# Performance work log

Hardware: AMD Instinct MI355X
Metric: run time of the kernel (lower is better)

Reference implementation:

```python
import jax, jax.numpy as jnp
import numpy as np

B = 16          # graphs per batch
N_PER = 1024    # coarse points per graph
M_PER = 4096    # fine (skip) points per graph
K = 3           # knn neighbors
NVEC = 64       # number of l=1 (vector) reps -> F = 3*NVEC
F = 3 * NVEC
F_SKIP = 64
HID = 256
OUT = 128
N = B * N_PER
M = B * M_PER


def _random_rotations(key, n):
    # QR of gaussian -> orthonormal local frames [n,3,3]
    q, _ = jnp.linalg.qr(jax.random.normal(key, (n, 3, 3), dtype=jnp.float32))
    return q


def setup_inputs() -> dict:
    key = jax.random.key(0)
    ks = jax.random.split(key, 10)
    x = jax.random.normal(ks[0], (N, F), dtype=jnp.float32)
    pos = jax.random.normal(ks[1], (N, 3), dtype=jnp.float32)
    pos_skip = jax.random.normal(ks[2], (M, 3), dtype=jnp.float32)
    x_skip = jax.random.normal(ks[3], (M, F_SKIP), dtype=jnp.float32)
    lframes = _random_rotations(ks[4], N)
    lframes_skip = _random_rotations(ks[5], M)
    W1 = jax.random.normal(ks[6], (F + F_SKIP, HID), dtype=jnp.float32) * 0.05
    b1 = jnp.zeros((HID,), dtype=jnp.float32)
    W2 = jax.random.normal(ks[7], (HID, OUT), dtype=jnp.float32) * 0.05
    b2 = jnp.zeros((OUT,), dtype=jnp.float32)
    batch = jnp.repeat(jnp.arange(B, dtype=jnp.int64), N_PER)
    batch_skip = jnp.repeat(jnp.arange(B, dtype=jnp.int64), M_PER)
    return dict(x=x, pos=pos, pos_skip=pos_skip, x_skip=x_skip,
                lframes=lframes, lframes_skip=lframes_skip,
                W1=W1, b1=b1, W2=W2, b2=b2,
                batch=batch, batch_skip=batch_skip)


def _knn_indices(pos, pos_skip):
    # Uniform per-example batching: knn of fine points (queries) among coarse points.
    px = pos.reshape(B, N_PER, 3)       # source points
    py = pos_skip.reshape(B, M_PER, 3)  # query points
    # squared distances via ||y||^2 + ||x||^2 - 2 y.x (only used for ranking)
    d2 = ((py * py).sum(-1)[:, :, None]
          + (px * px).sum(-1)[:, None, :]
          - 2.0 * jnp.einsum('bmd,bnd->bmn', py, px))  # [B, M_PER, N_PER]
    _, idx = jax.lax.top_k(-d2, K)                     # [B, M_PER, K] local indices
    # globalize indices (batch offset)
    x_idx = (idx + (jnp.arange(B) * N_PER)[:, None, None]).reshape(M, K)
    return x_idx


def reference(x, pos, pos_skip, x_skip, lframes, lframes_skip,
              W1, b1, W2, b2, batch, batch_skip):
    x_idx = _knn_indices(pos, pos_skip)                 # [M, K]

    # exact squared distances on gathered neighbors (matches torch diff*diff path)
    diff = pos[x_idx] - pos_skip[:, None, :]            # [M, K, 3]
    sqd = (diff * diff).sum(-1)                         # [M, K]
    w = 1.0 / jnp.maximum(sqd, 1e-16)                   # [M, K]

    # change of local frames: U = R_end @ R_start^T, per edge
    Rx = lframes[x_idx]                                 # [M, K, 3, 3]
    Ry = lframes_skip                                   # [M, 3, 3]
    U = jnp.einsum('mab,mkcb->mkac', Ry, Rx)            # [M, K, 3, 3]

    # transform features (NVEC vector reps) into the target frame
    xv = x[x_idx].reshape(M, K, NVEC, 3)                # gathered edge features
    xt = jnp.einsum('mkab,mkvb->mkva', U, xv)           # [M, K, NVEC, 3]

    # weighted mean over the K neighbors (== scatter-sum / scatter-sum, since
    # each target node has exactly K incoming edges)
    num = (xt * w[:, :, None, None]).sum(axis=1)        # [M, NVEC, 3]
    den = w.sum(axis=1)[:, None, None]                  # [M, 1, 1]
    y = (num / den).reshape(M, F)

    h = jnp.concatenate([y, x_skip], axis=-1)           # [M, F + F_SKIP]
    out = jax.nn.relu(h @ W1 + b1) @ W2 + b2            # [M, OUT]
    return (out, pos_skip, batch_skip, lframes_skip)
```

## Files before the change

### kernel.cpp

```cpp
#include <hip/hip_runtime.h>
#include <hip/hip_bf16.h>

#define B_GR   16
#define N_PER  1024
#define M_PER  4096
#define NVEC   64
#define FDIM   192
#define FSKIP  64
#define HID    256
#define ODIM   128
#define N_TOT  (B_GR * N_PER)
#define M_TOT  (B_GR * M_PER)

typedef __attribute__((ext_vector_type(8))) short short8v;
typedef __attribute__((ext_vector_type(4))) float f32x4;

__device__ __forceinline__ unsigned short f2bf(float f) {
    __hip_bfloat16 h = __float2bfloat16(f);
    return *reinterpret_cast<unsigned short*>(&h);
}

__device__ __forceinline__ int hsw(int r, int e) {
    return r * 256 + (e ^ ((r & 7) << 3));
}

__global__ __launch_bounds__(256) void prep_tail_kernel(
    const float* __restrict__ W1, const float* __restrict__ W2,
    const float* __restrict__ pos_skip,
    const int*   __restrict__ batch_skip,
    const float* __restrict__ lframes_skip,
    unsigned short* __restrict__ wt1, unsigned short* __restrict__ wt2,
    float* __restrict__ dst)
{
    const int i = blockIdx.x * 256 + threadIdx.x;
    if (i < 65536) {
        const int k = i >> 8, c = i & 255;
        wt1[c * 256 + k] = f2bf(W1[i]);
    } else if (i < 98304) {
        const int j = i - 65536;
        const int k = j >> 7, c = j & 127;
        wt2[c * 256 + k] = f2bf(W2[j]);
    } else {
        const int t = i - 98304;
        const int P = M_TOT * 3;
        const int Q = P + M_TOT;
        if (t < P)      dst[t] = pos_skip[t];
        else if (t < Q) dst[t] = (float)batch_skip[t - P];
        else            dst[t] = lframes_skip[t - Q];
    }
}

__global__ __launch_bounds__(512, 2) void fused_kernel(
    const float* __restrict__ x,
    const float* __restrict__ pos,
    const float* __restrict__ pos_skip,
    const float* __restrict__ x_skip,
    const float* __restrict__ lframes,
    const float* __restrict__ lframes_skip,
    const unsigned short* __restrict__ wt1,
    const float* __restrict__ b1,
    const unsigned short* __restrict__ wt2,
    const float* __restrict__ b2,
    float* __restrict__ out)
{
    __shared__ __align__(16) char smraw[64 * 256 * 2];
    __shared__ __align__(16) float Usc[64 * 28];
    __shared__ int idxL[64 * 3];

    float4*         pc = reinterpret_cast<float4*>(smraw);
    unsigned short* hb = reinterpret_cast<unsigned short*>(smraw);

    const int tid  = threadIdx.x;
    const int lane = tid & 63;
    const int wv   = tid >> 6;
    const int raw  = blockIdx.x;
    const int blk  = (raw & 7) * 128 + (raw >> 3);
    const int lo   = lane & 15;
    const int hi   = lane >> 4;
    const int b    = blk >> 6;

    #pragma unroll
    for (int k = 0; k < 2; ++k) {
        const int j = tid + k * 512;
        const float* p = pos + (size_t)(b * N_PER + j) * 3;
        float a0 = p[0], a1 = p[1], a2 = p[2];
        pc[j] = make_float4(a0, a1, a2, a0*a0 + a1*a1 + a2*a2);
    }
    __syncthreads();

    {
        const int q   = tid >> 3;
        const int sub = tid & 7;
        const int m   = blk * 64 + q;
        float nqx, nqy, nqz, qq;
        {
            const float qx = pos_skip[m*3+0], qy = pos_skip[m*3+1],
                        qz = pos_skip[m*3+2];
            qq  = qx*qx + qy*qy + qz*qz;
            nqx = -2.0f*qx; nqy = -2.0f*qy; nqz = -2.0f*qz;
        }

        float d0 = 1e30f, d1 = 1e30f, d2 = 1e30f;
        int   i0 = 0,     i1 = 0,     i2 = 0;
        #pragma unroll 4
        for (int t = 0; t < 128; ++t) {
            const int j = t*8 + sub;
            float4 c = pc[j];
            float r = fmaf(nqx, c.x, fmaf(nqy, c.y, fmaf(nqz, c.z, qq + c.w)));
            bool c0 = r < d0, c1 = r < d1, c2 = r < d2;
            i2 = c2 ? (c1 ? i1 : j) : i2;
            i1 = c1 ? (c0 ? i0 : j) : i1;
            i0 = c0 ? j : i0;
            d2 = c2 ? (c1 ? d1 : r) : d2;
            d1 = c1 ? (c0 ? d0 : r) : d1;
            d0 = c0 ? r : d0;
        }
        #pragma unroll
        for (int mask = 1; mask <= 4; mask <<= 1) {
            float e0 = __shfl_xor(d0, mask), e1 = __shfl_xor(d1, mask),
                  e2 = __shfl_xor(d2, mask);
            int   j0 = __shfl_xor(i0, mask), j1 = __shfl_xor(i1, mask),
                  j2 = __shfl_xor(i2, mask);
            const float ee[3] = {e0, e1, e2};
            const int   jj[3] = {j0, j1, j2};
            #pragma unroll
            for (int s = 0; s < 3; ++s) {
                const float e = ee[s]; const int j = jj[s];
                bool c0 = (e < d0) || (e == d0 && j < i0);
                bool c1 = (e < d1) || (e == d1 && j < i1);
                bool c2 = (e < d2) || (e == d2 && j < i2);
                i2 = c2 ? (c1 ? i1 : j) : i2;
                i1 = c1 ? (c0 ? i0 : j) : i1;
                i0 = c0 ? j : i0;
                d2 = c2 ? (c1 ? d1 : e) : d2;
                d1 = c1 ? (c0 ? d0 : e) : d1;
                d0 = c0 ? e : d0;
            }
        }

        if (sub < 3) {
            const int jl = (sub == 0) ? i0 : (sub == 1) ? i1 : i2;
            idxL[q*3 + sub] = jl;

            const float qx = -0.5f*nqx, qy = -0.5f*nqy, qz = -0.5f*nqz;
            float w[3];
            const int jls[3] = {i0, i1, i2};
            #pragma unroll
            for (int s = 0; s < 3; ++s) {
                float4 c = pc[jls[s]];
                float dx = c.x - qx, dy = c.y - qy, dz = c.z - qz;
                w[s] = 1.0f / fmaxf(dx*dx + dy*dy + dz*dz, 1e-16f);
            }
            const float wsub = (sub == 0) ? w[0] : (sub == 1) ? w[1] : w[2];
            const float sS   = wsub / (w[0] + w[1] + w[2]);
            const int   nb   = b * N_PER + jl;

            float RyS[9], Rx[9];
            #pragma unroll
            for (int t = 0; t < 9; ++t) RyS[t] = sS * lframes_skip[(size_t)m*9 + t];
            #pragma unroll
            for (int t = 0; t < 9; ++t) Rx[t] = lframes[(size_t)nb*9 + t];

            float* dst = &Usc[q*28 + sub*9];
            #pragma unroll
            for (int a = 0; a < 3; ++a)
                #pragma unroll
                for (int c = 0; c < 3; ++c)
                    dst[a*3+c] = RyS[a*3+0]*Rx[c*3+0]
                               + RyS[a*3+1]*Rx[c*3+1]
                               + RyS[a*3+2]*Rx[c*3+2];
        }
    }

    if (wv >= 4) {
        #pragma unroll
        for (int rr = 0; rr < 8; ++rr) {
            const int r = wv * 8 + rr;
            const int m = blk * 64 + r;
            hb[hsw(r, 192+lane)] = f2bf(x_skip[(size_t)m*FSKIP + lane]);
        }
    }
    __syncthreads();

    for (int rr = 0; rr < 8; ++rr) {
        const int r = wv * 8 + rr;
        const int m = blk * 64 + r;
        const int nbs[3] = {b*N_PER + idxL[r*3+0],
                            b*N_PER + idxL[r*3+1],
                            b*N_PER + idxL[r*3+2]};

        float Ub[28];
        float4* Ub4 = reinterpret_cast<float4*>(Ub);
        #pragma unroll
        for (int t = 0; t < 7; ++t)
            Ub4[t] = *reinterpret_cast<const float4*>(&Usc[r*28 + t*4]);

        float n0 = 0.f, n1 = 0.f, n2 = 0.f;
        #pragma unroll
        for (int k = 0; k < 3; ++k) {
            const float* xp = x + (size_t)nbs[k]*FDIM + lane*3;
            const float v0 = xp[0], v1 = xp[1], v2 = xp[2];
            const int o = k*9;
            n0 += Ub[o+0]*v0 + Ub[o+1]*v1 + Ub[o+2]*v2;
            n1 += Ub[o+3]*v0 + Ub[o+4]*v1 + Ub[o+5]*v2;
            n2 += Ub[o+6]*v0 + Ub[o+7]*v1 + Ub[o+8]*v2;
        }
        hb[hsw(r, lane*3+0)] = f2bf(n0);
        hb[hsw(r, lane*3+1)] = f2bf(n1);
        hb[hsw(r, lane*3+2)] = f2bf(n2);
        if (wv < 4)
            hb[hsw(r, 192+lane)] = f2bf(x_skip[(size_t)m*FSKIP + lane]);
    }
    __syncthreads();

    f32x4 acc[4][2];
    #pragma unroll
    for (int fi = 0; fi < 4; ++fi)
        #pragma unroll
        for (int ci = 0; ci < 2; ++ci) acc[fi][ci] = (f32x4)0.f;

    for (int ks = 0; ks < 8; ++ks) {
        const int kk = ks*32 + hi*8;
        short8v a[4], bf[2];
        #pragma unroll
        for (int fi = 0; fi < 4; ++fi) {
            const int r = fi*16 + lo;
            a[fi] = *reinterpret_cast<const short8v*>(
                &hb[r*256 + (kk ^ ((lo & 7) << 3))]);
        }
        #pragma unroll
        for (int ci = 0; ci < 2; ++ci) {
            const int cb = wv*32 + ci*16 + lo;
            bf[ci] = *reinterpret_cast<const short8v*>(&wt1[cb*256 + kk]);
        }
        #pragma unroll
        for (int fi = 0; fi < 4; ++fi)
            #pragma unroll
            for (int ci = 0; ci < 2; ++ci)
                acc[fi][ci] = __builtin_amdgcn_mfma_f32_16x16x32_bf16(
                    a[fi], bf[ci], acc[fi][ci], 0, 0, 0);
    }
    __syncthreads();

    {
        float b1v[2];
        #pragma unroll
        for (int ci = 0; ci < 2; ++ci) b1v[ci] = b1[wv*32 + ci*16 + lo];
        #pragma unroll
        for (int fi = 0; fi < 4; ++fi)
            #pragma unroll
            for (int ci = 0; ci < 2; ++ci)
                #pragma unroll
                for (int q = 0; q < 4; ++q) {
                    const int r = fi*16 + hi*4 + q;
                    const int c = wv*32 + ci*16 + lo;
                    hb[hsw(r, c)] = f2bf(fmaxf(acc[fi][ci][q] + b1v[ci], 0.f));
                }
    }
    __syncthreads();

    f32x4 acc2[4];
    #pragma unroll
    for (int fi = 0; fi < 4; ++fi) acc2[fi] = (f32x4)0.f;

    for (int ks = 0; ks < 8; ++ks) {
        const int kk = ks*32 + hi*8;
        short8v a[4], bf;
        #pragma unroll
        for (int fi = 0; fi < 4; ++fi) {
            const int r = fi*16 + lo;
            a[fi] = *reinterpret_cast<const short8v*>(
                &hb[r*256 + (kk ^ ((lo & 7) << 3))]);
        }
        {
            const int cb = wv*16 + lo;
            bf = *reinterpret_cast<const short8v*>(&wt2[cb*256 + kk]);
        }
        #pragma unroll
        for (int fi = 0; fi < 4; ++fi)
            acc2[fi] = __builtin_amdgcn_mfma_f32_16x16x32_bf16(
                a[fi], bf, acc2[fi], 0, 0, 0);
    }

    {
        const float b2v = b2[wv*16 + lo];
        #pragma unroll
        for (int fi = 0; fi < 4; ++fi)
            #pragma unroll
            for (int q = 0; q < 4; ++q) {
                const int r = fi*16 + hi*4 + q;
                const int c = wv*16 + lo;
                out[(size_t)(blk*64 + r)*ODIM + c] = acc2[fi][q] + b2v;
            }
    }
}

extern "C" void kernel_launch(void* const* d_in, const int* in_sizes, int n_in,
                              void* d_out, int out_size, void* d_ws, size_t ws_size,
                              hipStream_t stream) {
    const float* x            = (const float*)d_in[0];
    const float* pos          = (const float*)d_in[1];
    const float* pos_skip     = (const float*)d_in[2];
    const float* x_skip       = (const float*)d_in[3];
    const float* lframes      = (const float*)d_in[4];
    const float* lframes_skip = (const float*)d_in[5];
    const float* W1           = (const float*)d_in[6];
    const float* b1           = (const float*)d_in[7];
    const float* W2           = (const float*)d_in[8];
    const float* b2           = (const float*)d_in[9];
    const int*   batch_skip   = (const int*)d_in[11];

    char* ws = (char*)d_ws;
    unsigned short* wt1 = (unsigned short*)ws;
    unsigned short* wt2 = (unsigned short*)(ws + 131072);
    float* out  = (float*)d_out;
    float* tail = out + (size_t)M_TOT * ODIM;

    prep_tail_kernel<<<3712, 256, 0, stream>>>(W1, W2, pos_skip, batch_skip,
                                               lframes_skip, wt1, wt2, tail);

    fused_kernel<<<M_TOT/64, 512, 0, stream>>>(x, pos, pos_skip, x_skip,
                                               lframes, lframes_skip,
                                               wt1, b1, wt2, b2, out);
}
```

Measured before the change: 66.26 us.

## Split fused kernel into separate kNN and MLP kernels

The kNN search moves out of the fused kernel into its own kernel, which writes global neighbor indices to workspace. The MLP kernel reads those indices, recomputes the weights from global pos, and loads x_skip up front. The goal is to give each phase its own occupancy and register budget, with the kNN kernel declared for 4 blocks per CU. The cost is an extra launch, a round trip of the indices through global memory, and the loss of overlap between the two phases inside one block.

After: 78.79 us. 1.19x slower.

```diff
diff --git a/kernel.cpp b/kernel.cpp
--- a/kernel.cpp
+++ b/kernel.cpp
@@ -50,7 +50,81 @@
     }
 }
 
-__global__ __launch_bounds__(512, 2) void fused_kernel(
+__global__ __launch_bounds__(512, 4) void knn_kernel(
+    const float* __restrict__ pos,
+    const float* __restrict__ pos_skip,
+    int* __restrict__ idxb)
+{
+    __shared__ float4 pc[N_PER];
+    const int tid = threadIdx.x;
+    const int raw = blockIdx.x;
+    const int blk = (raw & 7) * 128 + (raw >> 3);
+    const int b   = blk >> 6;
+
+    #pragma unroll
+    for (int k = 0; k < 2; ++k) {
+        const int j = tid + k * 512;
+        const float* p = pos + (size_t)(b * N_PER + j) * 3;
+        float a0 = p[0], a1 = p[1], a2 = p[2];
+        pc[j] = make_float4(a0, a1, a2, a0*a0 + a1*a1 + a2*a2);
+    }
+    __syncthreads();
+
+    const int q   = tid >> 3;
+    const int sub = tid & 7;
+    const int m   = blk * 64 + q;
+    float nqx, nqy, nqz, qq;
+    {
+        const float qx = pos_skip[m*3+0], qy = pos_skip[m*3+1],
+                    qz = pos_skip[m*3+2];
+        qq  = qx*qx + qy*qy + qz*qz;
+        nqx = -2.0f*qx; nqy = -2.0f*qy; nqz = -2.0f*qz;
+    }
+
+    float d0 = 1e30f, d1 = 1e30f, d2 = 1e30f;
+    int   i0 = 0,     i1 = 0,     i2 = 0;
+    #pragma unroll 4
+    for (int t = 0; t < 128; ++t) {
+        const int j = t*8 + sub;
+        float4 c = pc[j];
+        float r = fmaf(nqx, c.x, fmaf(nqy, c.y, fmaf(nqz, c.z, qq + c.w)));
+        bool c0 = r < d0, c1 = r < d1, c2 = r < d2;
+        i2 = c2 ? (c1 ? i1 : j) : i2;
+        i1 = c1 ? (c0 ? i0 : j) : i1;
+        i0 = c0 ? j : i0;
+        d2 = c2 ? (c1 ? d1 : r) : d2;
+        d1 = c1 ? (c0 ? d0 : r) : d1;
+        d0 = c0 ? r : d0;
+    }
+    #pragma unroll
+    for (int mask = 1; mask <= 4; mask <<= 1) {
+        float e0 = __shfl_xor(d0, mask), e1 = __shfl_xor(d1, mask),
+              e2 = __shfl_xor(d2, mask);
+        int   j0 = __shfl_xor(i0, mask), j1 = __shfl_xor(i1, mask),
+              j2 = __shfl_xor(i2, mask);
+        const float ee[3] = {e0, e1, e2};
+        const int   jj[3] = {j0, j1, j2};
+        #pragma unroll
+        for (int s = 0; s < 3; ++s) {
+            const float e = ee[s]; const int j = jj[s];
+            bool c0 = (e < d0) || (e == d0 && j < i0);
+            bool c1 = (e < d1) || (e == d1 && j < i1);
+            bool c2 = (e < d2) || (e == d2 && j < i2);
+            i2 = c2 ? (c1 ? i1 : j) : i2;
+            i1 = c1 ? (c0 ? i0 : j) : i1;
+            i0 = c0 ? j : i0;
+            d2 = c2 ? (c1 ? d1 : e) : d2;
+            d1 = c1 ? (c0 ? d0 : e) : d1;
+            d0 = c0 ? e : d0;
+        }
+    }
+    if (sub < 3) {
+        const int jl = (sub == 0) ? i0 : (sub == 1) ? i1 : i2;
+        idxb[m*3 + sub] = b * N_PER + jl;
+    }
+}
+
+__global__ __launch_bounds__(512, 2) void mlp_kernel(
     const float* __restrict__ x,
     const float* __restrict__ pos,
     const float* __restrict__ pos_skip,
@@ -61,14 +135,11 @@
     const float* __restrict__ b1,
     const unsigned short* __restrict__ wt2,
     const float* __restrict__ b2,
+    const int*   __restrict__ idxb,
     float* __restrict__ out)
 {
-    __shared__ __align__(16) char smraw[64 * 256 * 2];
+    __shared__ __align__(16) unsigned short hb[64 * 256];
     __shared__ __align__(16) float Usc[64 * 28];
-    __shared__ int idxL[64 * 3];
-
-    float4*         pc = reinterpret_cast<float4*>(smraw);
-    unsigned short* hb = reinterpret_cast<unsigned short*>(smraw);
 
     const int tid  = threadIdx.x;
     const int lane = tid & 63;
@@ -80,80 +151,30 @@
     const int b    = blk >> 6;
 
     #pragma unroll
-    for (int k = 0; k < 2; ++k) {
-        const int j = tid + k * 512;
-        const float* p = pos + (size_t)(b * N_PER + j) * 3;
-        float a0 = p[0], a1 = p[1], a2 = p[2];
-        pc[j] = make_float4(a0, a1, a2, a0*a0 + a1*a1 + a2*a2);
-    }
-    __syncthreads();
+    for (int rr = 0; rr < 8; ++rr) {
+        const int r = wv * 8 + rr;
+        const int m = blk * 64 + r;
+        hb[hsw(r, 192+lane)] = f2bf(x_skip[(size_t)m*FSKIP + lane]);
+    }
 
     {
-        const int q   = tid >> 3;
-        const int sub = tid & 7;
-        const int m   = blk * 64 + q;
-        float nqx, nqy, nqz, qq;
-        {
+        const int q = tid >> 3, sub = tid & 7;
+        if (sub < 3) {
+            const int m  = blk * 64 + q;
+            const int j0 = idxb[m*3+0], j1 = idxb[m*3+1], j2 = idxb[m*3+2];
             const float qx = pos_skip[m*3+0], qy = pos_skip[m*3+1],
                         qz = pos_skip[m*3+2];
-            qq  = qx*qx + qy*qy + qz*qz;
-            nqx = -2.0f*qx; nqy = -2.0f*qy; nqz = -2.0f*qz;
-        }
-
-        float d0 = 1e30f, d1 = 1e30f, d2 = 1e30f;
-        int   i0 = 0,     i1 = 0,     i2 = 0;
-        #pragma unroll 4
-        for (int t = 0; t < 128; ++t) {
-            const int j = t*8 + sub;
-            float4 c = pc[j];
-            float r = fmaf(nqx, c.x, fmaf(nqy, c.y, fmaf(nqz, c.z, qq + c.w)));
-            bool c0 = r < d0, c1 = r < d1, c2 = r < d2;
-            i2 = c2 ? (c1 ? i1 : j) : i2;
-            i1 = c1 ? (c0 ? i0 : j) : i1;
-            i0 = c0 ? j : i0;
-            d2 = c2 ? (c1 ? d1 : r) : d2;
-            d1 = c1 ? (c0 ? d0 : r) : d1;
-            d0 = c0 ? r : d0;
-        }
-        #pragma unroll
-        for (int mask = 1; mask <= 4; mask <<= 1) {
-            float e0 = __shfl_xor(d0, mask), e1 = __shfl_xor(d1, mask),
-                  e2 = __shfl_xor(d2, mask);
-            int   j0 = __shfl_xor(i0, mask), j1 = __shfl_xor(i1, mask),
-                  j2 = __shfl_xor(i2, mask);
-            const float ee[3] = {e0, e1, e2};
-            const int   jj[3] = {j0, j1, j2};
+            float w[3];
+            const int jls[3] = {j0, j1, j2};
             #pragma unroll
             for (int s = 0; s < 3; ++s) {
-                const float e = ee[s]; const int j = jj[s];
-                bool c0 = (e < d0) || (e == d0 && j < i0);
-                bool c1 = (e < d1) || (e == d1 && j < i1);
-                bool c2 = (e < d2) || (e == d2 && j < i2);
-                i2 = c2 ? (c1 ? i1 : j) : i2;
-                i1 = c1 ? (c0 ? i0 : j) : i1;
-                i0 = c0 ? j : i0;
-                d2 = c2 ? (c1 ? d1 : e) : d2;
-                d1 = c1 ? (c0 ? d0 : e) : d1;
-                d0 = c0 ? e : d0;
-            }
-        }
-
-        if (sub < 3) {
-            const int jl = (sub == 0) ? i0 : (sub == 1) ? i1 : i2;
-            idxL[q*3 + sub] = jl;
-
-            const float qx = -0.5f*nqx, qy = -0.5f*nqy, qz = -0.5f*nqz;
-            float w[3];
-            const int jls[3] = {i0, i1, i2};
-            #pragma unroll
-            for (int s = 0; s < 3; ++s) {
-                float4 c = pc[jls[s]];
-                float dx = c.x - qx, dy = c.y - qy, dz = c.z - qz;
+                const float* pp = pos + (size_t)jls[s] * 3;
+                float dx = pp[0]-qx, dy = pp[1]-qy, dz = pp[2]-qz;
                 w[s] = 1.0f / fmaxf(dx*dx + dy*dy + dz*dz, 1e-16f);
             }
             const float wsub = (sub == 0) ? w[0] : (sub == 1) ? w[1] : w[2];
             const float sS   = wsub / (w[0] + w[1] + w[2]);
-            const int   nb   = b * N_PER + jl;
+            const int   nb   = (sub == 0) ? j0 : (sub == 1) ? j1 : j2;
 
             float RyS[9], Rx[9];
             #pragma unroll
@@ -171,23 +192,12 @@
                                + RyS[a*3+2]*Rx[c*3+2];
         }
     }
-
-    if (wv >= 4) {
-        #pragma unroll
-        for (int rr = 0; rr < 8; ++rr) {
-            const int r = wv * 8 + rr;
-            const int m = blk * 64 + r;
-            hb[hsw(r, 192+lane)] = f2bf(x_skip[(size_t)m*FSKIP + lane]);
-        }
-    }
     __syncthreads();
 
     for (int rr = 0; rr < 8; ++rr) {
         const int r = wv * 8 + rr;
         const int m = blk * 64 + r;
-        const int nbs[3] = {b*N_PER + idxL[r*3+0],
-                            b*N_PER + idxL[r*3+1],
-                            b*N_PER + idxL[r*3+2]};
+        const int nbs[3] = {idxb[m*3+0], idxb[m*3+1], idxb[m*3+2]};
 
         float Ub[28];
         float4* Ub4 = reinterpret_cast<float4*>(Ub);
@@ -208,8 +218,6 @@
         hb[hsw(r, lane*3+0)] = f2bf(n0);
         hb[hsw(r, lane*3+1)] = f2bf(n1);
         hb[hsw(r, lane*3+2)] = f2bf(n2);
-        if (wv < 4)
-            hb[hsw(r, 192+lane)] = f2bf(x_skip[(size_t)m*FSKIP + lane]);
     }
     __syncthreads();
 
@@ -311,15 +319,18 @@
     const int*   batch_skip   = (const int*)d_in[11];
 
     char* ws = (char*)d_ws;
-    unsigned short* wt1 = (unsigned short*)ws;
-    unsigned short* wt2 = (unsigned short*)(ws + 131072);
+    unsigned short* wt1  = (unsigned short*)ws;
+    unsigned short* wt2  = (unsigned short*)(ws + 131072);
+    int*            idxb = (int*)(ws + 131072 + 65536);
     float* out  = (float*)d_out;
     float* tail = out + (size_t)M_TOT * ODIM;
 
     prep_tail_kernel<<<3712, 256, 0, stream>>>(W1, W2, pos_skip, batch_skip,
                                                lframes_skip, wt1, wt2, tail);
 
-    fused_kernel<<<M_TOT/64, 512, 0, stream>>>(x, pos, pos_skip, x_skip,
-                                               lframes, lframes_skip,
-                                               wt1, b1, wt2, b2, out);
-}
+    knn_kernel<<<M_TOT/64, 512, 0, stream>>>(pos, pos_skip, idxb);
+
+    mlp_kernel<<<M_TOT/64, 512, 0, stream>>>(x, pos, pos_skip, x_skip,
+                                             lframes, lframes_skip,
+                                             wt1, b1, wt2, b2, idxb, out);
+}
```
